# Performance work log

Measured on AMD Instinct MI355X. Metric: run time of the kernel, lower is better.

## Reference

```python
import jax, jax.numpy as jnp
import numpy as np

DIM = 128
HEADS = 4
DIM_HEAD = 32
HIDDEN = HEADS * DIM_HEAD  # 128
SCALE = DIM_HEAD ** -0.5


def setup_inputs() -> dict:
    key = jax.random.key(0)
    k1, k2, k3, k4 = jax.random.split(key, 4)
    x = jax.random.normal(k1, (2, DIM, 16, 64, 64), dtype=jnp.float32)
    # conv2d 1x1 weights == channel matmuls
    Wqkv = jax.random.normal(k2, (3 * HIDDEN, DIM), dtype=jnp.float32) * (DIM ** -0.5)
    Wout = jax.random.normal(k3, (DIM, HIDDEN), dtype=jnp.float32) * (HIDDEN ** -0.5)
    bout = jax.random.normal(k4, (DIM,), dtype=jnp.float32) * 0.01
    return {"x": x, "Wqkv": Wqkv, "Wout": Wout, "bout": bout}


def reference(x, Wqkv, Wout, bout):
    b, c, f, h, w = x.shape
    n = h * w
    # 'b c f h w -> (b f) c (h w)'
    xf = jnp.transpose(x, (0, 2, 1, 3, 4)).reshape(b * f, c, n)
    # 1x1 conv == channel projection
    qkv = jnp.einsum('oc,bcn->bon', Wqkv, xf)  # (bf, 3*hidden, n)
    q, k, v = jnp.split(qkv, 3, axis=1)
    def to_heads(t):
        return t.reshape(b * f, HEADS, DIM_HEAD, n)  # 'b (h c) n -> b h c n'
    q, k, v = to_heads(q), to_heads(k), to_heads(v)
    q = jax.nn.softmax(q, axis=-2) * SCALE   # softmax over dim_head axis
    k = jax.nn.softmax(k, axis=-1)           # softmax over spatial axis
    v = v / n
    # context: (bf, h, d, e); out: (bf, h, e, n)
    context = jnp.einsum('bhdn,bhen->bhde', k, v)
    out = jnp.einsum('bhde,bhdn->bhen', context, q)
    out = out.reshape(b * f, HIDDEN, n)      # '(h c) merge'
    out = jnp.einsum('oc,bcn->bon', Wout, out) + bout[None, :, None]
    # '(b f) c (h w) -> b c f h w'
    out = out.reshape(b, f, c, h, w).transpose(0, 2, 1, 3, 4)
    return out
```

## Files before the change

### kernel.cpp

```cpp
#include <hip/hip_runtime.h>


constexpr float kSCALE = 0.17677669529663687f;

typedef __attribute__((ext_vector_type(8))) short short8;
typedef __attribute__((ext_vector_type(4))) float f32x4;

__device__ __forceinline__ float bfu2f(unsigned int u) {
  union { unsigned int i; float f; } c; c.i = u << 16; return c.f;
}
__device__ __forceinline__ unsigned short f2bf(float f) {
  union { float f; unsigned int i; } c; c.f = f;
  unsigned int r = c.i + 0x7fffu + ((c.i >> 16) & 1u);
  return (unsigned short)(r >> 16);
}
__device__ __forceinline__ void pack8(const float* v, unsigned short* dst16) {
  union { unsigned short u[8]; uint4 q; } t;
  #pragma unroll
  for (int i = 0; i < 8; ++i) t.u[i] = f2bf(v[i]);
  *(uint4*)dst16 = t.q;
}
__device__ __forceinline__ int swz(int row, int col) { return row * 128 + (col ^ ((row & 7) << 3)); }

__global__ __launch_bounds__(256) void k_wconv(const float* __restrict__ W,
                                               unsigned short* __restrict__ Wbf) {
  const int i = (blockIdx.x * 256 + threadIdx.x) * 4;
  const float4 v = *(const float4*)&W[i];
  union { unsigned short u[4]; uint2 q; } t;
  t.u[0] = f2bf(v.x); t.u[1] = f2bf(v.y); t.u[2] = f2bf(v.z); t.u[3] = f2bf(v.w);
  *(uint2*)&Wbf[i] = t.q;
}

__global__ __launch_bounds__(512) void k_fqkv(const float* __restrict__ x,
                                              const unsigned short* __restrict__ Wbf,
                                              unsigned short* __restrict__ qsm,
                                              float* __restrict__ ctx,
                                              float* __restrict__ sumexp) {
  __shared__ __align__(16) char smem[65536];
  unsigned short* R0 = (unsigned short*)smem;
  unsigned short* R1 = (unsigned short*)(smem + 32768);
  const int ntile = blockIdx.x, fr = blockIdx.y;
  const int bb = fr >> 4, ff = fr & 15;
  const int tid = threadIdx.x;
  const float* xfr = x + ((size_t)bb * 2048 + ff) * 4096;

  {
    const int nn = tid & 127, cq = tid >> 7;
    const int ng = ntile * 128 + nn;
    #pragma unroll
    for (int p = 0; p < 4; ++p) {
      const int c8 = cq * 4 + p;
      float v[8];
      #pragma unroll
      for (int j = 0; j < 8; ++j) v[j] = xfr[(size_t)(c8 * 8 + j) * 65536 + ng];
      pack8(v, &R0[swz(nn, c8 * 8)]);
    }
  }
  __syncthreads();

  const int l = tid & 63, w = tid >> 6;
  const int wo = (w >> 1) * 96, wn = (w & 1) * 64;
  const int lr = l & 15, lg = l >> 4;
  f32x4 acc[6][4];
  #pragma unroll
  for (int i = 0; i < 6; ++i)
    #pragma unroll
    for (int j = 0; j < 4; ++j) acc[i][j] = 0.f;

  #pragma unroll
  for (int ks = 0; ks < 4; ++ks) {
    const int k0 = ks * 32 + lg * 8;
    short8 a[6], b[4];
    #pragma unroll
    for (int i = 0; i < 6; ++i) a[i] = *(const short8*)&Wbf[(size_t)(wo + 16 * i + lr) * 128 + k0];
    #pragma unroll
    for (int j = 0; j < 4; ++j) b[j] = *(const short8*)&R0[swz(wn + 16 * j + lr, k0)];
    #pragma unroll
    for (int i = 0; i < 6; ++i)
      #pragma unroll
      for (int j = 0; j < 4; ++j)
        acc[i][j] = __builtin_amdgcn_mfma_f32_16x16x32_bf16(a[i], b[j], acc[i][j], 0, 0, 0);
  }

  #pragma unroll
  for (int i = 0; i < 6; ++i) {
    const int grow = wo + 16 * i;
    if (grow < 128) {
      #pragma unroll
      for (int j = 0; j < 4; ++j) {
        const int n = wn + 16 * j + lr, o4 = grow + 4 * lg;
        union { unsigned short u[4]; uint2 q; } t;
        #pragma unroll
        for (int r = 0; r < 4; ++r) t.u[r] = f2bf(acc[i][j][r]);
        *(uint2*)&R1[n * 128 + (o4 ^ ((n & 7) << 3))] = t.q;
      }
    }
  }
  __syncthreads();

  #pragma unroll
  for (int i = 0; i < 6; ++i) {
    const int grow = wo + 16 * i;
    if (grow >= 128 && grow < 256) {
      #pragma unroll
      for (int j = 0; j < 4; ++j) {
        const int n = wn + 16 * j + lr;
        #pragma unroll
        for (int r = 0; r < 4; ++r) {
          const int dd = grow - 128 + 4 * lg + r;
          R0[dd * 128 + (n ^ ((dd & 7) << 3))] = f2bf(__expf(acc[i][j][r]));
        }
      }
    }
  }
  {
    const int n = tid & 127, h = tid >> 7;
    float v[32];
    #pragma unroll
    for (int m = 0; m < 4; ++m) {
      const uint4 u = *(const uint4*)&R1[n * 128 + ((h * 32 + m * 8) ^ ((n & 7) << 3))];
      v[m*8+0] = bfu2f(u.x & 0xffffu); v[m*8+1] = bfu2f(u.x >> 16);
      v[m*8+2] = bfu2f(u.y & 0xffffu); v[m*8+3] = bfu2f(u.y >> 16);
      v[m*8+4] = bfu2f(u.z & 0xffffu); v[m*8+5] = bfu2f(u.z >> 16);
      v[m*8+6] = bfu2f(u.w & 0xffffu); v[m*8+7] = bfu2f(u.w >> 16);
    }
    float mx = v[0];
    #pragma unroll
    for (int d = 1; d < 32; ++d) mx = fmaxf(mx, v[d]);
    float s = 0.f;
    #pragma unroll
    for (int d = 0; d < 32; ++d) { v[d] = __expf(v[d] - mx); s += v[d]; }
    const float inv = 1.f / s;
    #pragma unroll
    for (int d = 0; d < 32; ++d) v[d] *= inv;
    unsigned short* qb = qsm + ((size_t)fr * 4096 + ntile * 128 + n) * 128 + h * 32;
    #pragma unroll
    for (int m = 0; m < 4; ++m) pack8(&v[m * 8], &qb[m * 8]);
  }
  __syncthreads();

  #pragma unroll
  for (int i = 0; i < 6; ++i) {
    const int grow = wo + 16 * i;
    if (grow >= 256) {
      #pragma unroll
      for (int j = 0; j < 4; ++j) {
        const int n = wn + 16 * j + lr;
        #pragma unroll
        for (int r = 0; r < 4; ++r) {
          const int e = grow - 256 + 4 * lg + r;
          R1[e * 128 + (n ^ ((e & 7) << 3))] = f2bf(acc[i][j][r]);
        }
      }
    }
  }
  __syncthreads();

  if (w < 4) {
    const int h = w;
    f32x4 c2[2][2];
    c2[0][0] = 0.f; c2[0][1] = 0.f; c2[1][0] = 0.f; c2[1][1] = 0.f;
    #pragma unroll
    for (int ks = 0; ks < 4; ++ks) {
      const int k0 = ks * 32 + lg * 8;
      short8 a2[2], b2[2];
      #pragma unroll
      for (int i2 = 0; i2 < 2; ++i2) a2[i2] = *(const short8*)&R0[swz(h * 32 + 16 * i2 + lr, k0)];
      #pragma unroll
      for (int j2 = 0; j2 < 2; ++j2) b2[j2] = *(const short8*)&R1[swz(h * 32 + 16 * j2 + lr, k0)];
      #pragma unroll
      for (int i2 = 0; i2 < 2; ++i2)
        #pragma unroll
        for (int j2 = 0; j2 < 2; ++j2)
          c2[i2][j2] = __builtin_amdgcn_mfma_f32_16x16x32_bf16(a2[i2], b2[j2], c2[i2][j2], 0, 0, 0);
    }
    float* cp = ctx + ((size_t)fr * 4 + h) * 1024;
    #pragma unroll
    for (int i2 = 0; i2 < 2; ++i2)
      #pragma unroll
      for (int j2 = 0; j2 < 2; ++j2)
        #pragma unroll
        for (int r = 0; r < 4; ++r)
          atomicAdd(&cp[(16 * i2 + 4 * lg + r) * 32 + 16 * j2 + lr], c2[i2][j2][r]);
  } else {
    const int h = w - 4;
    const int dd = l & 31, half = l >> 5;
    const int row = h * 32 + dd;
    float s = 0.f;
    #pragma unroll
    for (int m = 0; m < 8; ++m) {
      const uint4 u = *(const uint4*)&R0[row * 128 + ((half * 64 + m * 8) ^ ((row & 7) << 3))];
      s += bfu2f(u.x & 0xffffu) + bfu2f(u.x >> 16) + bfu2f(u.y & 0xffffu) + bfu2f(u.y >> 16)
         + bfu2f(u.z & 0xffffu) + bfu2f(u.z >> 16) + bfu2f(u.w & 0xffffu) + bfu2f(u.w >> 16);
    }
    s += __shfl_xor(s, 32);
    if (half == 0) atomicAdd(&sumexp[fr * 128 + row], s);
  }
}

__global__ __launch_bounds__(256) void k_mbuild(const float* __restrict__ Wout,
                                                const float* __restrict__ ctx,
                                                const float* __restrict__ sumexp,
                                                unsigned short* __restrict__ Mbf) {
  __shared__ float Wo[128][129];
  __shared__ float cn[4][32][33];
  const int fr = blockIdx.x, tid = threadIdx.x;
  {
    int o = tid >> 5; const int c4 = (tid & 31) * 4;
    #pragma unroll
    for (int p = 0; p < 16; ++p, o += 8) {
      const float4 w = *(const float4*)&Wout[o * 128 + c4];
      Wo[o][c4] = w.x; Wo[o][c4 + 1] = w.y; Wo[o][c4 + 2] = w.z; Wo[o][c4 + 3] = w.w;
    }
  }
  for (int i = tid; i < 4096; i += 256) {
    const int h = i >> 10, dd = (i >> 5) & 31, e = i & 31;
    const float s = sumexp[fr * 128 + h * 32 + dd];
    cn[h][dd][e] = ctx[(((size_t)fr * 4 + h) * 32 + dd) * 32 + e] * (kSCALE / (4096.f * s));
  }
  __syncthreads();
  const int c = tid & 127, hc = c >> 5, dc = c & 31;
  for (int o = tid >> 7; o < 128; o += 2) {
    float s = 0.f;
    #pragma unroll
    for (int e = 0; e < 32; ++e) s = fmaf(Wo[o][hc * 32 + e], cn[hc][dc][e], s);
    Mbf[(size_t)fr * 16384 + o * 128 + c] = f2bf(s);
  }
}

__global__ __launch_bounds__(256) void k_out(const unsigned short* __restrict__ qsm,
                                             const unsigned short* __restrict__ Mbf,
                                             const float* __restrict__ bout,
                                             float* __restrict__ out) {
  __shared__ __align__(16) char smem[67584];
  unsigned short* Ap = (unsigned short*)smem;
  unsigned short* Bp = (unsigned short*)(smem + 32768);
  float* Ob = (float*)smem;
  const int ntile = blockIdx.x, fr = blockIdx.y;
  const int bb = fr >> 4, ff = fr & 15;
  const int tid = threadIdx.x;
  {
    const int c8 = (tid & 15) * 8;
    int o = tid >> 4;
    const unsigned short* Mf = Mbf + (size_t)fr * 16384;
    #pragma unroll
    for (int p = 0; p < 8; ++p, o += 16) {
      uint4 qv = *(const uint4*)&Mf[o * 128 + c8];
      *(uint4*)&Ap[swz(o, c8)] = qv;
    }
  }
  {
    const int c8 = (tid & 15) * 8;
    int n = tid >> 4;
    const unsigned short* qb = qsm + ((size_t)fr * 4096 + ntile * 128) * 128;
    #pragma unroll
    for (int p = 0; p < 8; ++p, n += 16) {
      uint4 qv = *(const uint4*)&qb[n * 128 + c8];
      *(uint4*)&Bp[swz(n, c8)] = qv;
    }
  }
  __syncthreads();

  const int l = tid & 63, w = tid >> 6;
  const int wo = (w >> 1) * 64, wn = (w & 1) * 64;
  const int lr = l & 15, lg = l >> 4;
  f32x4 acc[4][4];
  #pragma unroll
  for (int i = 0; i < 4; ++i)
    #pragma unroll
    for (int j = 0; j < 4; ++j) acc[i][j] = 0.f;

  #pragma unroll
  for (int ks = 0; ks < 4; ++ks) {
    const int k0 = ks * 32 + lg * 8;
    short8 a[4], b[4];
    #pragma unroll
    for (int i = 0; i < 4; ++i) a[i] = *(const short8*)&Ap[swz(wo + 16 * i + lr, k0)];
    #pragma unroll
    for (int j = 0; j < 4; ++j) b[j] = *(const short8*)&Bp[swz(wn + 16 * j + lr, k0)];
    #pragma unroll
    for (int i = 0; i < 4; ++i)
      #pragma unroll
      for (int j = 0; j < 4; ++j)
        acc[i][j] = __builtin_amdgcn_mfma_f32_16x16x32_bf16(a[i], b[j], acc[i][j], 0, 0, 0);
  }
  __syncthreads();

  #pragma unroll
  for (int i = 0; i < 4; ++i) {
    #pragma unroll
    for (int j = 0; j < 4; ++j) {
      const int n = wn + 16 * j + lr;
      #pragma unroll
      for (int r = 0; r < 4; ++r) {
        const int o = wo + 16 * i + 4 * lg + r;
        Ob[o * 132 + n] = acc[i][j][r] + bout[o];
      }
    }
  }
  __syncthreads();
  {
    float* ofr = out + ((size_t)bb * 2048 + ff) * 4096;
    const int m = tid & 15;
    #pragma unroll
    for (int p = 0; p < 8; ++p) {
      const int o = p * 16 + (tid >> 4);
      float4 v0 = *(const float4*)&Ob[o * 132 + m * 4];
      float4 v1 = *(const float4*)&Ob[o * 132 + 64 + m * 4];
      *(float4*)&ofr[(size_t)o * 65536 + ntile * 128 + m * 4] = v0;
      *(float4*)&ofr[(size_t)o * 65536 + ntile * 128 + 64 + m * 4] = v1;
    }
  }
}

extern "C" void kernel_launch(void* const* d_in, const int* in_sizes, int n_in,
                              void* d_out, int out_size, void* d_ws, size_t ws_size,
                              hipStream_t stream) {
  const float* x    = (const float*)d_in[0];
  const float* Wqkv = (const float*)d_in[1];
  const float* Wout = (const float*)d_in[2];
  const float* bout = (const float*)d_in[3];
  float* out = (float*)d_out;

  char* ws = (char*)d_ws;
  unsigned short* qsm = (unsigned short*)ws;
  float* ctxb   = (float*)(ws + 33554432u);
  float* sumexp = (float*)(ws + 33554432u + 524288u);
  unsigned short* Mbf = (unsigned short*)(ws + 34095104u);
  unsigned short* Wbf = (unsigned short*)(ws + 35143680u);

  hipMemsetAsync(ctxb, 0, 524288u + 16384u, stream);

  k_wconv<<<dim3(48), 256, 0, stream>>>(Wqkv, Wbf);
  k_fqkv<<<dim3(32, 32), 512, 0, stream>>>(x, Wbf, qsm, ctxb, sumexp);
  k_mbuild<<<dim3(32), 256, 0, stream>>>(Wout, ctxb, sumexp, Mbf);
  k_out<<<dim3(32, 32), 256, 0, stream>>>(qsm, Mbf, bout, out);
}
```

Before: 199.4 us.

## Halve fqkv tile, write partial contexts instead of atomics, restructure mbuild and out

The fused QKV kernel now processes 64 spatial positions per block, doubling the grid. It computes the q softmax directly in registers with cross-lane shuffles instead of staging through shared memory. Context and exp-sum partials are written per tile to a larger workspace rather than atomically accumulated, which removes the memset. k_mbuild is split per head and performs the reduction over the 64 partials. k_out reads M directly from global memory and writes the output straight from registers, skipping the LDS transpose, so its stores are less coalesced and the workspace reads grow.

```diff
diff --git a/kernel.cpp b/kernel.cpp
--- a/kernel.cpp
+++ b/kernel.cpp
@@ -20,7 +20,6 @@
   for (int i = 0; i < 8; ++i) t.u[i] = f2bf(v[i]);
   *(uint4*)dst16 = t.q;
 }
-__device__ __forceinline__ int swz(int row, int col) { return row * 128 + (col ^ ((row & 7) << 3)); }
 
 __global__ __launch_bounds__(256) void k_wconv(const float* __restrict__ W,
                                                unsigned short* __restrict__ Wbf) {
@@ -31,232 +30,245 @@
   *(uint2*)&Wbf[i] = t.q;
 }
 
-__global__ __launch_bounds__(512) void k_fqkv(const float* __restrict__ x,
-                                              const unsigned short* __restrict__ Wbf,
-                                              unsigned short* __restrict__ qsm,
-                                              float* __restrict__ ctx,
-                                              float* __restrict__ sumexp) {
-  __shared__ __align__(16) char smem[65536];
-  unsigned short* R0 = (unsigned short*)smem;
-  unsigned short* R1 = (unsigned short*)(smem + 32768);
+__global__ __launch_bounds__(512, 4) void k_fqkv(const float* __restrict__ x,
+                                                 const unsigned short* __restrict__ Wbf,
+                                                 unsigned short* __restrict__ qsm,
+                                                 float* __restrict__ ctxp,
+                                                 float* __restrict__ sexp) {
+  __shared__ __align__(16) unsigned short R0[64 * 128];
+  __shared__ __align__(16) unsigned short EK[128 * 64];
+  __shared__ __align__(16) unsigned short VV[128 * 64];
   const int ntile = blockIdx.x, fr = blockIdx.y;
   const int bb = fr >> 4, ff = fr & 15;
   const int tid = threadIdx.x;
   const float* xfr = x + ((size_t)bb * 2048 + ff) * 4096;
 
   {
-    const int nn = tid & 127, cq = tid >> 7;
-    const int ng = ntile * 128 + nn;
-    #pragma unroll
-    for (int p = 0; p < 4; ++p) {
-      const int c8 = cq * 4 + p;
+    const int nn = tid & 63, cg = tid >> 6;
+    const int ng = ntile * 64 + nn;
+    #pragma unroll
+    for (int p = 0; p < 2; ++p) {
+      const int c8 = cg * 2 + p;
       float v[8];
       #pragma unroll
       for (int j = 0; j < 8; ++j) v[j] = xfr[(size_t)(c8 * 8 + j) * 65536 + ng];
-      pack8(v, &R0[swz(nn, c8 * 8)]);
+      pack8(v, &R0[nn * 128 + ((c8 * 8) ^ ((nn & 7) << 3))]);
     }
   }
   __syncthreads();
 
   const int l = tid & 63, w = tid >> 6;
-  const int wo = (w >> 1) * 96, wn = (w & 1) * 64;
+  const int wo = (w >> 1) * 96, wn = (w & 1) * 32;
   const int lr = l & 15, lg = l >> 4;
-  f32x4 acc[6][4];
-  #pragma unroll
-  for (int i = 0; i < 6; ++i)
-    #pragma unroll
-    for (int j = 0; j < 4; ++j) acc[i][j] = 0.f;
+  f32x4 acc[6][2];
+  #pragma unroll
+  for (int i = 0; i < 6; ++i) { acc[i][0] = 0.f; acc[i][1] = 0.f; }
 
   #pragma unroll
   for (int ks = 0; ks < 4; ++ks) {
     const int k0 = ks * 32 + lg * 8;
-    short8 a[6], b[4];
+    short8 a[6], b[2];
     #pragma unroll
     for (int i = 0; i < 6; ++i) a[i] = *(const short8*)&Wbf[(size_t)(wo + 16 * i + lr) * 128 + k0];
     #pragma unroll
-    for (int j = 0; j < 4; ++j) b[j] = *(const short8*)&R0[swz(wn + 16 * j + lr, k0)];
+    for (int j = 0; j < 2; ++j) {
+      const int n = wn + 16 * j + lr;
+      b[j] = *(const short8*)&R0[n * 128 + (k0 ^ ((n & 7) << 3))];
+    }
     #pragma unroll
     for (int i = 0; i < 6; ++i)
       #pragma unroll
-      for (int j = 0; j < 4; ++j)
+      for (int j = 0; j < 2; ++j)
         acc[i][j] = __builtin_amdgcn_mfma_f32_16x16x32_bf16(a[i], b[j], acc[i][j], 0, 0, 0);
   }
-
-  #pragma unroll
-  for (int i = 0; i < 6; ++i) {
-    const int grow = wo + 16 * i;
-    if (grow < 128) {
-      #pragma unroll
-      for (int j = 0; j < 4; ++j) {
-        const int n = wn + 16 * j + lr, o4 = grow + 4 * lg;
-        union { unsigned short u[4]; uint2 q; } t;
-        #pragma unroll
-        for (int r = 0; r < 4; ++r) t.u[r] = f2bf(acc[i][j][r]);
-        *(uint2*)&R1[n * 128 + (o4 ^ ((n & 7) << 3))] = t.q;
-      }
-    }
-  }
-  __syncthreads();
 
   #pragma unroll
   for (int i = 0; i < 6; ++i) {
     const int grow = wo + 16 * i;
     if (grow >= 128 && grow < 256) {
       #pragma unroll
-      for (int j = 0; j < 4; ++j) {
+      for (int j = 0; j < 2; ++j) {
         const int n = wn + 16 * j + lr;
         #pragma unroll
         for (int r = 0; r < 4; ++r) {
           const int dd = grow - 128 + 4 * lg + r;
-          R0[dd * 128 + (n ^ ((dd & 7) << 3))] = f2bf(__expf(acc[i][j][r]));
+          EK[dd * 64 + (n ^ ((dd & 7) << 3))] = f2bf(__expf(acc[i][j][r]));
         }
       }
-    }
-  }
-  {
-    const int n = tid & 127, h = tid >> 7;
-    float v[32];
-    #pragma unroll
-    for (int m = 0; m < 4; ++m) {
-      const uint4 u = *(const uint4*)&R1[n * 128 + ((h * 32 + m * 8) ^ ((n & 7) << 3))];
-      v[m*8+0] = bfu2f(u.x & 0xffffu); v[m*8+1] = bfu2f(u.x >> 16);
-      v[m*8+2] = bfu2f(u.y & 0xffffu); v[m*8+3] = bfu2f(u.y >> 16);
-      v[m*8+4] = bfu2f(u.z & 0xffffu); v[m*8+5] = bfu2f(u.z >> 16);
-      v[m*8+6] = bfu2f(u.w & 0xffffu); v[m*8+7] = bfu2f(u.w >> 16);
-    }
-    float mx = v[0];
-    #pragma unroll
-    for (int d = 1; d < 32; ++d) mx = fmaxf(mx, v[d]);
-    float s = 0.f;
-    #pragma unroll
-    for (int d = 0; d < 32; ++d) { v[d] = __expf(v[d] - mx); s += v[d]; }
-    const float inv = 1.f / s;
-    #pragma unroll
-    for (int d = 0; d < 32; ++d) v[d] *= inv;
-    unsigned short* qb = qsm + ((size_t)fr * 4096 + ntile * 128 + n) * 128 + h * 32;
-    #pragma unroll
-    for (int m = 0; m < 4; ++m) pack8(&v[m * 8], &qb[m * 8]);
-  }
-  __syncthreads();
-
-  #pragma unroll
-  for (int i = 0; i < 6; ++i) {
-    const int grow = wo + 16 * i;
-    if (grow >= 256) {
-      #pragma unroll
-      for (int j = 0; j < 4; ++j) {
+    } else if (grow >= 256) {
+      #pragma unroll
+      for (int j = 0; j < 2; ++j) {
         const int n = wn + 16 * j + lr;
         #pragma unroll
         for (int r = 0; r < 4; ++r) {
           const int e = grow - 256 + 4 * lg + r;
-          R1[e * 128 + (n ^ ((e & 7) << 3))] = f2bf(acc[i][j][r]);
+          VV[e * 64 + (n ^ ((e & 7) << 3))] = f2bf(acc[i][j][r]);
         }
       }
     }
   }
-  __syncthreads();
-
+  #pragma unroll
+  for (int i0 = 0; i0 < 6; i0 += 2) {
+    const int grow0 = wo + 16 * i0;
+    if (grow0 < 128) {
+      const int h = grow0 >> 5;
+      #pragma unroll
+      for (int j = 0; j < 2; ++j) {
+        const int n = wn + 16 * j + lr;
+        float v0[4], v1[4];
+        float m = -1e30f;
+        #pragma unroll
+        for (int r = 0; r < 4; ++r) {
+          v0[r] = acc[i0][j][r]; v1[r] = acc[i0 + 1][j][r];
+          m = fmaxf(m, fmaxf(v0[r], v1[r]));
+        }
+        m = fmaxf(m, __shfl_xor(m, 16));
+        m = fmaxf(m, __shfl_xor(m, 32));
+        float s = 0.f;
+        #pragma unroll
+        for (int r = 0; r < 4; ++r) {
+          v0[r] = __expf(v0[r] - m); v1[r] = __expf(v1[r] - m);
+          s += v0[r] + v1[r];
+        }
+        s += __shfl_xor(s, 16);
+        s += __shfl_xor(s, 32);
+        const float inv = 1.f / s;
+        union { unsigned short u[4]; uint2 q; } t0, t1;
+        #pragma unroll
+        for (int r = 0; r < 4; ++r) { t0.u[r] = f2bf(v0[r] * inv); t1.u[r] = f2bf(v1[r] * inv); }
+        unsigned short* qb = qsm + ((size_t)fr * 4096 + ntile * 64 + n) * 128 + h * 32 + 4 * lg;
+        *(uint2*)&qb[0]  = t0.q;
+        *(uint2*)&qb[16] = t1.q;
+      }
+    }
+  }
+  __syncthreads();
+
+  const int bp = fr * 64 + ntile;
   if (w < 4) {
     const int h = w;
     f32x4 c2[2][2];
     c2[0][0] = 0.f; c2[0][1] = 0.f; c2[1][0] = 0.f; c2[1][1] = 0.f;
     #pragma unroll
-    for (int ks = 0; ks < 4; ++ks) {
+    for (int ks = 0; ks < 2; ++ks) {
       const int k0 = ks * 32 + lg * 8;
       short8 a2[2], b2[2];
       #pragma unroll
-      for (int i2 = 0; i2 < 2; ++i2) a2[i2] = *(const short8*)&R0[swz(h * 32 + 16 * i2 + lr, k0)];
-      #pragma unroll
-      for (int j2 = 0; j2 < 2; ++j2) b2[j2] = *(const short8*)&R1[swz(h * 32 + 16 * j2 + lr, k0)];
+      for (int i2 = 0; i2 < 2; ++i2) {
+        const int row = h * 32 + 16 * i2 + lr;
+        a2[i2] = *(const short8*)&EK[row * 64 + (k0 ^ ((row & 7) << 3))];
+      }
+      #pragma unroll
+      for (int j2 = 0; j2 < 2; ++j2) {
+        const int row = h * 32 + 16 * j2 + lr;
+        b2[j2] = *(const short8*)&VV[row * 64 + (k0 ^ ((row & 7) << 3))];
+      }
       #pragma unroll
       for (int i2 = 0; i2 < 2; ++i2)
         #pragma unroll
         for (int j2 = 0; j2 < 2; ++j2)
           c2[i2][j2] = __builtin_amdgcn_mfma_f32_16x16x32_bf16(a2[i2], b2[j2], c2[i2][j2], 0, 0, 0);
     }
-    float* cp = ctx + ((size_t)fr * 4 + h) * 1024;
+    float* cp = ctxp + ((size_t)bp * 4 + h) * 1024;
     #pragma unroll
     for (int i2 = 0; i2 < 2; ++i2)
       #pragma unroll
       for (int j2 = 0; j2 < 2; ++j2)
         #pragma unroll
         for (int r = 0; r < 4; ++r)
-          atomicAdd(&cp[(16 * i2 + 4 * lg + r) * 32 + 16 * j2 + lr], c2[i2][j2][r]);
+          cp[(16 * i2 + 4 * lg + r) * 32 + 16 * j2 + lr] = c2[i2][j2][r];
   } else {
     const int h = w - 4;
-    const int dd = l & 31, half = l >> 5;
-    const int row = h * 32 + dd;
+    const int rl = l & 31, half = l >> 5;
+    const int row = h * 32 + rl;
     float s = 0.f;
     #pragma unroll
-    for (int m = 0; m < 8; ++m) {
-      const uint4 u = *(const uint4*)&R0[row * 128 + ((half * 64 + m * 8) ^ ((row & 7) << 3))];
+    for (int m = 0; m < 4; ++m) {
+      const int ng = (half * 32 + m * 8) ^ ((row & 7) << 3);
+      const uint4 u = *(const uint4*)&EK[row * 64 + ng];
       s += bfu2f(u.x & 0xffffu) + bfu2f(u.x >> 16) + bfu2f(u.y & 0xffffu) + bfu2f(u.y >> 16)
          + bfu2f(u.z & 0xffffu) + bfu2f(u.z >> 16) + bfu2f(u.w & 0xffffu) + bfu2f(u.w >> 16);
     }
     s += __shfl_xor(s, 32);
-    if (half == 0) atomicAdd(&sumexp[fr * 128 + row], s);
+    if (half == 0) sexp[(size_t)bp * 128 + row] = s;
   }
 }
 
 __global__ __launch_bounds__(256) void k_mbuild(const float* __restrict__ Wout,
-                                                const float* __restrict__ ctx,
-                                                const float* __restrict__ sumexp,
+                                                const float* __restrict__ ctxp,
+                                                const float* __restrict__ sexp,
                                                 unsigned short* __restrict__ Mbf) {
-  __shared__ float Wo[128][129];
-  __shared__ float cn[4][32][33];
-  const int fr = blockIdx.x, tid = threadIdx.x;
-  {
-    int o = tid >> 5; const int c4 = (tid & 31) * 4;
-    #pragma unroll
-    for (int p = 0; p < 16; ++p, o += 8) {
-      const float4 w = *(const float4*)&Wout[o * 128 + c4];
-      Wo[o][c4] = w.x; Wo[o][c4 + 1] = w.y; Wo[o][c4 + 2] = w.z; Wo[o][c4 + 3] = w.w;
-    }
-  }
-  for (int i = tid; i < 4096; i += 256) {
-    const int h = i >> 10, dd = (i >> 5) & 31, e = i & 31;
-    const float s = sumexp[fr * 128 + h * 32 + dd];
-    cn[h][dd][e] = ctx[(((size_t)fr * 4 + h) * 32 + dd) * 32 + e] * (kSCALE / (4096.f * s));
-  }
-  __syncthreads();
-  const int c = tid & 127, hc = c >> 5, dc = c & 31;
-  for (int o = tid >> 7; o < 128; o += 2) {
+  __shared__ float Wo[128][33];
+  __shared__ float cn[32][36];
+  __shared__ float ses[32];
+  const int h = blockIdx.x, fr = blockIdx.y, tid = threadIdx.x;
+
+  float4 c4 = make_float4(0.f, 0.f, 0.f, 0.f);
+  {
+    const float* base = ctxp + ((size_t)fr * 64) * 4096 + h * 1024 + tid * 4;
+    #pragma unroll 8
+    for (int p = 0; p < 64; ++p) {
+      const float4 v = *(const float4*)&base[(size_t)p * 4096];
+      c4.x += v.x; c4.y += v.y; c4.z += v.z; c4.w += v.w;
+    }
+  }
+  if (tid < 32) {
     float s = 0.f;
-    #pragma unroll
-    for (int e = 0; e < 32; ++e) s = fmaf(Wo[o][hc * 32 + e], cn[hc][dc][e], s);
-    Mbf[(size_t)fr * 16384 + o * 128 + c] = f2bf(s);
-  }
-}
-
-__global__ __launch_bounds__(256) void k_out(const unsigned short* __restrict__ qsm,
-                                             const unsigned short* __restrict__ Mbf,
-                                             const float* __restrict__ bout,
-                                             float* __restrict__ out) {
-  __shared__ __align__(16) char smem[67584];
-  unsigned short* Ap = (unsigned short*)smem;
-  unsigned short* Bp = (unsigned short*)(smem + 32768);
-  float* Ob = (float*)smem;
+    const float* sb = sexp + ((size_t)fr * 64) * 128 + h * 32 + tid;
+    #pragma unroll 8
+    for (int p = 0; p < 64; ++p) s += sb[(size_t)p * 128];
+    ses[tid] = s;
+  }
+  {
+    const int o = tid >> 1, e0 = (tid & 1) * 16;
+    #pragma unroll
+    for (int q = 0; q < 4; ++q) {
+      const float4 v = *(const float4*)&Wout[o * 128 + h * 32 + e0 + 4 * q];
+      Wo[o][e0 + 4 * q] = v.x; Wo[o][e0 + 4 * q + 1] = v.y;
+      Wo[o][e0 + 4 * q + 2] = v.z; Wo[o][e0 + 4 * q + 3] = v.w;
+    }
+  }
+  __syncthreads();
+  {
+    const int dd = tid >> 3, e0 = (tid & 7) * 4;
+    const float sc = kSCALE / (4096.f * ses[dd]);
+    cn[dd][e0] = c4.x * sc; cn[dd][e0 + 1] = c4.y * sc;
+    cn[dd][e0 + 2] = c4.z * sc; cn[dd][e0 + 3] = c4.w * sc;
+  }
+  __syncthreads();
+  {
+    const int o = tid >> 1, dbase = (tid & 1) * 16;
+    union { unsigned short u[16]; uint4 q[2]; } t;
+    #pragma unroll
+    for (int dq = 0; dq < 16; ++dq) {
+      const int dc = dbase + dq;
+      float s = 0.f;
+      #pragma unroll
+      for (int e = 0; e < 32; ++e) s = fmaf(Wo[o][e], cn[dc][e], s);
+      t.u[dq] = f2bf(s);
+    }
+    unsigned short* mb = Mbf + (size_t)fr * 16384 + o * 128 + h * 32 + dbase;
+    *(uint4*)&mb[0] = t.q[0];
+    *(uint4*)&mb[8] = t.q[1];
+  }
+}
+
+__global__ __launch_bounds__(256, 4) void k_out(const unsigned short* __restrict__ qsm,
+                                                const unsigned short* __restrict__ Mbf,
+                                                const float* __restrict__ bout,
+                                                float* __restrict__ out) {
+  __shared__ __align__(16) unsigned short Bp[128 * 128];
   const int ntile = blockIdx.x, fr = blockIdx.y;
   const int bb = fr >> 4, ff = fr & 15;
   const int tid = threadIdx.x;
   {
     const int c8 = (tid & 15) * 8;
-    int o = tid >> 4;
-    const unsigned short* Mf = Mbf + (size_t)fr * 16384;
-    #pragma unroll
-    for (int p = 0; p < 8; ++p, o += 16) {
-      uint4 qv = *(const uint4*)&Mf[o * 128 + c8];
-      *(uint4*)&Ap[swz(o, c8)] = qv;
-    }
-  }
-  {
-    const int c8 = (tid & 15) * 8;
     int n = tid >> 4;
     const unsigned short* qb = qsm + ((size_t)fr * 4096 + ntile * 128) * 128;
     #pragma unroll
     for (int p = 0; p < 8; ++p, n += 16) {
-      uint4 qv = *(const uint4*)&qb[n * 128 + c8];
-      *(uint4*)&Bp[swz(n, c8)] = qv;
+      const uint4 qv = *(const uint4*)&qb[n * 128 + c8];
+      *(uint4*)&Bp[n * 128 + (c8 ^ ((n & 7) << 3))] = qv;
     }
   }
   __syncthreads();
@@ -270,45 +282,37 @@
     #pragma unroll
     for (int j = 0; j < 4; ++j) acc[i][j] = 0.f;
 
+  const unsigned short* Mf = Mbf + (size_t)fr * 16384;
   #pragma unroll
   for (int ks = 0; ks < 4; ++ks) {
     const int k0 = ks * 32 + lg * 8;
     short8 a[4], b[4];
     #pragma unroll
-    for (int i = 0; i < 4; ++i) a[i] = *(const short8*)&Ap[swz(wo + 16 * i + lr, k0)];
-    #pragma unroll
-    for (int j = 0; j < 4; ++j) b[j] = *(const short8*)&Bp[swz(wn + 16 * j + lr, k0)];
+    for (int i = 0; i < 4; ++i) a[i] = *(const short8*)&Mf[(wo + 16 * i + lr) * 128 + k0];
+    #pragma unroll
+    for (int j = 0; j < 4; ++j) {
+      const int n = wn + 16 * j + lr;
+      b[j] = *(const short8*)&Bp[n * 128 + (k0 ^ ((n & 7) << 3))];
+    }
     #pragma unroll
     for (int i = 0; i < 4; ++i)
       #pragma unroll
       for (int j = 0; j < 4; ++j)
         acc[i][j] = __builtin_amdgcn_mfma_f32_16x16x32_bf16(a[i], b[j], acc[i][j], 0, 0, 0);
   }
-  __syncthreads();
-
+
+  float* ofr = out + ((size_t)bb * 2048 + ff) * 4096;
   #pragma unroll
   for (int i = 0; i < 4; ++i) {
+    const int o0 = wo + 16 * i + 4 * lg;
+    const float4 bo = *(const float4*)&bout[o0];
     #pragma unroll
     for (int j = 0; j < 4; ++j) {
-      const int n = wn + 16 * j + lr;
-      #pragma unroll
-      for (int r = 0; r < 4; ++r) {
-        const int o = wo + 16 * i + 4 * lg + r;
-        Ob[o * 132 + n] = acc[i][j][r] + bout[o];
-      }
-    }
-  }
-  __syncthreads();
-  {
-    float* ofr = out + ((size_t)bb * 2048 + ff) * 4096;
-    const int m = tid & 15;
-    #pragma unroll
-    for (int p = 0; p < 8; ++p) {
-      const int o = p * 16 + (tid >> 4);
-      float4 v0 = *(const float4*)&Ob[o * 132 + m * 4];
-      float4 v1 = *(const float4*)&Ob[o * 132 + 64 + m * 4];
-      *(float4*)&ofr[(size_t)o * 65536 + ntile * 128 + m * 4] = v0;
-      *(float4*)&ofr[(size_t)o * 65536 + ntile * 128 + 64 + m * 4] = v1;
+      const int n = ntile * 128 + wn + 16 * j + lr;
+      ofr[(size_t)(o0 + 0) * 65536 + n] = acc[i][j][0] + bo.x;
+      ofr[(size_t)(o0 + 1) * 65536 + n] = acc[i][j][1] + bo.y;
+      ofr[(size_t)(o0 + 2) * 65536 + n] = acc[i][j][2] + bo.z;
+      ofr[(size_t)(o0 + 3) * 65536 + n] = acc[i][j][3] + bo.w;
     }
   }
 }
@@ -324,15 +328,13 @@
 
   char* ws = (char*)d_ws;
   unsigned short* qsm = (unsigned short*)ws;
-  float* ctxb   = (float*)(ws + 33554432u);
-  float* sumexp = (float*)(ws + 33554432u + 524288u);
-  unsigned short* Mbf = (unsigned short*)(ws + 34095104u);
-  unsigned short* Wbf = (unsigned short*)(ws + 35143680u);
-
-  hipMemsetAsync(ctxb, 0, 524288u + 16384u, stream);
+  float* ctxp  = (float*)(ws + 33554432u);
+  float* sexp  = (float*)(ws + 67108864u);
+  unsigned short* Mbf = (unsigned short*)(ws + 68157440u);
+  unsigned short* Wbf = (unsigned short*)(ws + 69206016u);
 
   k_wconv<<<dim3(48), 256, 0, stream>>>(Wqkv, Wbf);
-  k_fqkv<<<dim3(32, 32), 512, 0, stream>>>(x, Wbf, qsm, ctxb, sumexp);
-  k_mbuild<<<dim3(32), 256, 0, stream>>>(Wout, ctxb, sumexp, Mbf);
+  k_fqkv<<<dim3(64, 32), 512, 0, stream>>>(x, Wbf, qsm, ctxp, sexp);
+  k_mbuild<<<dim3(4, 32), 256, 0, stream>>>(Wout, ctxp, sexp, Mbf);
   k_out<<<dim3(32, 32), 256, 0, stream>>>(qsm, Mbf, bout, out);
 }
```

Result: no change. 201.1 us (+0.8%).
